# Performance work log

Measured on AMD Instinct MI355X. Metric: run time of the kernel, lower is better.

The kernel has to match this reference:

```python
import jax, jax.numpy as jnp
import numpy as np

B, C, H, W, NH = 8, 192, 128, 128, 6  # batch, channels, height, width, heads


def setup_inputs() -> dict:
    key = jax.random.key(0)
    ks = jax.random.split(key, 5)
    return {
        "x": jax.random.normal(ks[0], (B, C, H, W), jnp.float32),
        "w_qkv": jax.random.normal(ks[1], (3 * C, 1, 3, 3), jnp.float32) * 0.1,  # grouped conv, groups=C
        "b_qkv": jax.random.normal(ks[2], (3 * C,), jnp.float32) * 0.1,
        "temperature": jnp.ones((NH, 1, 1), jnp.float32),
        "w_out": jax.random.normal(ks[3], (C, C), jnp.float32) * 0.05,  # 1x1 conv as dense
        "b_out": jax.random.normal(ks[4], (C,), jnp.float32) * 0.05,
    }


def reference(x, w_qkv, b_qkv, temperature, w_out, b_out):
    b, c, h, w = x.shape
    nh = temperature.shape[0]
    # grouped 3x3 conv (groups = in_ch), padding=1
    qkv = jax.lax.conv_general_dilated(
        x, w_qkv, window_strides=(1, 1), padding=[(1, 1), (1, 1)],
        feature_group_count=c, dimension_numbers=("NCHW", "OIHW", "NCHW"),
    ) + b_qkv[None, :, None, None]
    q, k, v = jnp.split(qkv, 3, axis=1)  # each [b, c, h, w]

    def to_heads(t):
        return t.reshape(b, nh, c // nh, h * w)  # b head c (h w)

    q, k, v = to_heads(q), to_heads(k), to_heads(v)
    eps = 1e-12  # F.normalize default
    q = q / jnp.maximum(jnp.linalg.norm(q, axis=-1, keepdims=True), eps)
    k = k / jnp.maximum(jnp.linalg.norm(k, axis=-1, keepdims=True), eps)
    attn = jnp.einsum("bhcn,bhdn->bhcd", q, k) * temperature[None]  # [b, nh, c/nh, c/nh]
    attn = jax.nn.softmax(attn, axis=-1)
    out = jnp.einsum("bhcd,bhdn->bhcn", attn, v).reshape(b, c, h, w)
    out = jnp.einsum("oc,bchw->bohw", w_out, out) + b_out[None, :, None, None]
    return out
```

## Files before the change

kernel.cpp:

```cpp
#include <hip/hip_runtime.h>
#include <hip/hip_bf16.h>

constexpr int B   = 8;
constexpr int Cc  = 192;
constexpr int H   = 128;
constexpr int Wd  = 128;
constexpr int NH  = 6;
constexpr int HW  = H * Wd;
constexpr int QKV = 3 * Cc;

typedef short s16x4 __attribute__((ext_vector_type(4)));
typedef short s16x8 __attribute__((ext_vector_type(8)));
typedef float f32x16 __attribute__((ext_vector_type(16)));

constexpr size_t OFF_QKV  = 0;
constexpr size_t OFF_ATTN = 150994944ULL;
constexpr size_t OFF_SSQ  = OFF_ATTN + 196608ULL;
constexpr size_t OFF_M    = OFF_SSQ + 12288ULL;
constexpr int    N_ZERO   = (196608 + 12288) / 4;

__device__ inline unsigned short f2bf(float f) {
    __hip_bfloat16 h = __float2bfloat16(f);
    return *(unsigned short*)&h;
}

__global__ void zero_kernel(float* __restrict__ p, int n) {
    int i = blockIdx.x * 256 + threadIdx.x;
    if (i < n) p[i] = 0.f;
}

constexpr int TS = 16;

__global__ __launch_bounds__(256) void conv_qkv(
    const float* __restrict__ x, const float* __restrict__ w,
    const float* __restrict__ bias, unsigned short* __restrict__ qkv,
    float* __restrict__ ssq)
{
    int tile = blockIdx.x;
    int g    = blockIdx.y;
    int b    = blockIdx.z;
    int tid  = threadIdx.x;
    int y    = tile * TS + (tid >> 4);
    int xq   = (tid & 15) * 8;

    const float* xp = x + ((size_t)b * Cc + g) * HW;

    float r[3][10];
    for (int dr = 0; dr < 3; ++dr) {
        int yy = y - 1 + dr;
        bool vy = (yy >= 0) && (yy < H);
        const float* rp = xp + (size_t)yy * Wd;
        if (vy) {
            float4 a4 = *(const float4*)(rp + xq);
            float4 b4 = *(const float4*)(rp + xq + 4);
            r[dr][0] = (xq > 0)   ? rp[xq - 1] : 0.f;
            r[dr][1] = a4.x; r[dr][2] = a4.y; r[dr][3] = a4.z; r[dr][4] = a4.w;
            r[dr][5] = b4.x; r[dr][6] = b4.y; r[dr][7] = b4.z; r[dr][8] = b4.w;
            r[dr][9] = (xq < 120) ? rp[xq + 8] : 0.f;
        } else {
            for (int i = 0; i < 10; ++i) r[dr][i] = 0.f;
        }
    }

    float wreg[3][9], breg[3];
    for (int j = 0; j < 3; ++j) {
        const float* wp = w + (size_t)(3 * g + j) * 9;
        for (int t = 0; t < 9; ++t) wreg[j][t] = wp[t];
        breg[j] = bias[3 * g + j];
    }

    bool track = (g < 128);
    float ss[3] = {0.f, 0.f, 0.f};

    for (int j = 0; j < 3; ++j) {
        unsigned short pk[8];
        for (int xx = 0; xx < 8; ++xx) {
            float s = breg[j];
            for (int dr = 0; dr < 3; ++dr)
                s += wreg[j][dr * 3 + 0] * r[dr][xx]
                   + wreg[j][dr * 3 + 1] * r[dr][xx + 1]
                   + wreg[j][dr * 3 + 2] * r[dr][xx + 2];
            if (track) ss[j] += s * s;
            pk[xx] = f2bf(s);
        }
        unsigned short* op = qkv + ((size_t)b * QKV + 3 * g + j) * HW
                                 + (size_t)y * Wd + xq;
        uint4 uu;
        uu.x = (unsigned int)pk[0] | ((unsigned int)pk[1] << 16);
        uu.y = (unsigned int)pk[2] | ((unsigned int)pk[3] << 16);
        uu.z = (unsigned int)pk[4] | ((unsigned int)pk[5] << 16);
        uu.w = (unsigned int)pk[6] | ((unsigned int)pk[7] << 16);
        *(uint4*)op = uu;
    }

    if (track) {
        __shared__ float red[256];
        for (int j = 0; j < 3; ++j) {
            red[tid] = ss[j];
            __syncthreads();
            for (int st = 128; st > 0; st >>= 1) {
                if (tid < st) red[tid] += red[tid + st];
                __syncthreads();
            }
            if (tid == 0) {
                int o = 3 * g + j;
                atomicAdd(&ssq[(o < Cc ? 0 : 1) * B * Cc + b * Cc + (o % Cc)], red[0]);
            }
            __syncthreads();
        }
    }
}

constexpr int NSEG = 64;
constexpr int SEGN = HW / NSEG;

__global__ __launch_bounds__(256) void qk_mfma(
    const unsigned short* __restrict__ qkv, float* __restrict__ attn)
{
    int h = blockIdx.y, b = blockIdx.z;
    int tid = threadIdx.x;
    int wv = tid >> 6, lane = tid & 63;
    int seg = blockIdx.x * 4 + wv;
    int col = lane & 31, half = lane >> 5;

    __shared__ float sred[4][1024];

    const unsigned short* qp = qkv + ((size_t)b * QKV + h * 32 + col) * HW
                                   + seg * SEGN + half * 8;
    const unsigned short* kp = qp + (size_t)Cc * HW;

    f32x16 acc0, acc1;
    for (int i = 0; i < 16; ++i) { acc0[i] = 0.f; acc1[i] = 0.f; }

    for (int kk = 0; kk < SEGN; kk += 32) {
        s16x8 a0 = *(const s16x8*)(qp + kk);
        s16x8 b0 = *(const s16x8*)(kp + kk);
        acc0 = __builtin_amdgcn_mfma_f32_32x32x16_bf16(a0, b0, acc0, 0, 0, 0);
        s16x8 a1 = *(const s16x8*)(qp + kk + 16);
        s16x8 b1 = *(const s16x8*)(kp + kk + 16);
        acc1 = __builtin_amdgcn_mfma_f32_32x32x16_bf16(a1, b1, acc1, 0, 0, 0);
    }

    int rb = half * 4;
    for (int r = 0; r < 16; ++r) {
        int row = (r & 3) + 8 * (r >> 2) + rb;
        sred[wv][row * 32 + col] = acc0[r] + acc1[r];
    }
    __syncthreads();
    float* ap = attn + (size_t)(b * NH + h) * 1024;
    for (int i = tid; i < 1024; i += 256)
        atomicAdd(&ap[i], sred[0][i] + sred[1][i] + sred[2][i] + sred[3][i]);
}

__global__ void softmax_attn(float* __restrict__ attn,
                             const float* __restrict__ ssq,
                             const float* __restrict__ temp)
{
    int h = blockIdx.x % NH, b = blockIdx.x / NH;
    __shared__ float nk[32];
    if (threadIdx.x < 32)
        nk[threadIdx.x] = fmaxf(sqrtf(ssq[B * Cc + b * Cc + h * 32 + threadIdx.x]), 1e-12f);
    __syncthreads();
    int c = threadIdx.x;
    if (c >= 32) return;
    float nq = fmaxf(sqrtf(ssq[b * Cc + h * 32 + c]), 1e-12f);
    float t = temp[h];
    float* ap = attn + ((size_t)(b * NH + h) * 32 + c) * 32;
    float row[32];
    float mx = -1e30f;
    for (int d = 0; d < 32; ++d) {
        float v = ap[d] / (nq * nk[d]) * t;
        row[d] = v;
        mx = fmaxf(mx, v);
    }
    float sum = 0.f;
    for (int d = 0; d < 32; ++d) { row[d] = expf(row[d] - mx); sum += row[d]; }
    float inv = 1.f / sum;
    for (int d = 0; d < 32; ++d) ap[d] = row[d] * inv;
}

__global__ __launch_bounds__(256) void make_m(
    const float* __restrict__ attn, const float* __restrict__ w_out,
    unsigned short* __restrict__ M)
{
    int h = blockIdx.x, b = blockIdx.y;
    __shared__ float as[32][33];
    for (int i = threadIdx.x; i < 1024; i += 256)
        as[i / 32][i % 32] = attn[(size_t)((b * NH + h) * 32 + i / 32) * 32 + i % 32];
    __syncthreads();
    for (int i = threadIdx.x; i < Cc * 32; i += 256) {
        int o = i / 32, d = i % 32;
        const float* wp = w_out + (size_t)o * Cc + h * 32;
        float s = 0.f;
        for (int cp = 0; cp < 32; ++cp) s += wp[cp] * as[cp][d];
        M[((size_t)b * Cc + o) * Cc + h * 32 + d] = f2bf(s);
    }
}

constexpr int BN = 128;

__global__ __launch_bounds__(256) void out_gemm(
    const unsigned short* __restrict__ M, const unsigned short* __restrict__ qkv,
    const float* __restrict__ b_out, float* __restrict__ out)
{
    int tid  = threadIdx.x;
    int wv   = tid >> 6, lane = tid & 63;
    int b    = blockIdx.y;
    int n0   = blockIdx.x * BN + wv * 32;
    int col  = lane & 31, half = lane >> 5;
    int a    = lane >> 3;
    int bq   = lane & 7;

    __shared__ unsigned short vsT[4][32][20];
    unsigned short (*vt)[20] = vsT[wv];

    const unsigned short* vp = qkv + ((size_t)b * QKV + 2 * Cc) * HW + n0 + 4 * bq;
    const unsigned short* mp = M + (size_t)b * Cc * Cc;

    f32x16 acc[6];
    for (int t = 0; t < 6; ++t)
        for (int i = 0; i < 16; ++i) acc[t][i] = 0.f;

    const unsigned short* s0 = vp + (size_t)(2 * a) * HW;
    ushort4 va = *(const ushort4*)s0;
    ushort4 vb = *(const ushort4*)(s0 + HW);

    for (int k0 = 0; k0 < Cc; k0 += 16) {
        *(unsigned int*)&vt[4 * bq + 0][2 * a] = (unsigned int)va.x | ((unsigned int)vb.x << 16);
        *(unsigned int*)&vt[4 * bq + 1][2 * a] = (unsigned int)va.y | ((unsigned int)vb.y << 16);
        *(unsigned int*)&vt[4 * bq + 2][2 * a] = (unsigned int)va.z | ((unsigned int)vb.z << 16);
        *(unsigned int*)&vt[4 * bq + 3][2 * a] = (unsigned int)va.w | ((unsigned int)vb.w << 16);
        if (k0 + 16 < Cc) {
            const unsigned short* s1 = vp + (size_t)(k0 + 16 + 2 * a) * HW;
            va = *(const ushort4*)s1;
            vb = *(const ushort4*)(s1 + HW);
        }
        __builtin_amdgcn_wave_barrier();
        s16x4 lo = *(const s16x4*)&vt[col][half * 8];
        s16x4 hi = *(const s16x4*)&vt[col][half * 8 + 4];
        s16x8 bf = __builtin_shufflevector(lo, hi, 0, 1, 2, 3, 4, 5, 6, 7);
        for (int mt = 0; mt < 6; ++mt) {
            s16x8 af = *(const s16x8*)(mp + (size_t)(mt * 32 + col) * Cc + k0 + half * 8);
            acc[mt] = __builtin_amdgcn_mfma_f32_32x32x16_bf16(af, bf, acc[mt], 0, 0, 0);
        }
        __builtin_amdgcn_wave_barrier();
    }

    for (int mt = 0; mt < 6; ++mt) {
        f32x16 c = acc[mt];
        for (int rr = 0; rr < 16; ++rr) {
            int row = (rr & 3) + 8 * (rr >> 2) + 4 * half;
            int o = mt * 32 + row;
            out[((size_t)b * Cc + o) * HW + n0 + col] = c[rr] + b_out[o];
        }
    }
}

extern "C" void kernel_launch(void* const* d_in, const int* in_sizes, int n_in,
                              void* d_out, int out_size, void* d_ws, size_t ws_size,
                              hipStream_t stream) {
    const float* x      = (const float*)d_in[0];
    const float* w_qkv  = (const float*)d_in[1];
    const float* b_qkv  = (const float*)d_in[2];
    const float* temp   = (const float*)d_in[3];
    const float* w_out  = (const float*)d_in[4];
    const float* b_out  = (const float*)d_in[5];
    float* out = (float*)d_out;

    char* ws = (char*)d_ws;
    unsigned short* qkv = (unsigned short*)(ws + OFF_QKV);
    float* attn         = (float*)(ws + OFF_ATTN);
    float* ssq          = (float*)(ws + OFF_SSQ);
    unsigned short* M   = (unsigned short*)(ws + OFF_M);

    zero_kernel<<<(N_ZERO + 255) / 256, 256, 0, stream>>>(attn, N_ZERO);
    conv_qkv<<<dim3(H / TS, Cc, B), 256, 0, stream>>>(x, w_qkv, b_qkv, qkv, ssq);
    qk_mfma<<<dim3(NSEG / 4, NH, B), 256, 0, stream>>>(qkv, attn);
    softmax_attn<<<B * NH, 64, 0, stream>>>(attn, ssq, temp);
    make_m<<<dim3(NH, B), 256, 0, stream>>>(attn, w_out, M);
    out_gemm<<<dim3(HW / BN, B), 256, 0, stream>>>(M, qkv, b_out, out);
}
```

Measured before the change: 298.9 us.

## Stage conv input in shared memory and replace QK atomics with partial buffers

The depthwise conv now loads a haloed 18x128 tile into shared memory with coalesced float4 loads and gets the left and right neighbour columns through lane shuffles. The sum-of-squares reduction switches from a shared-memory tree with many barriers to wavefront shuffle reductions, with one atomic per wave. The QK^T kernel stages Q and K chunks in LDS with coalesced loads and writes per-partition partial results instead of atomics, and softmax sums the 8 partials. This adds a barrier per chunk in the QK kernel and cuts its grid to 8 blocks per (b,h), which may reduce parallelism.

```diff
diff --git a/kernel.cpp b/kernel.cpp
--- a/kernel.cpp
+++ b/kernel.cpp
@@ -14,10 +14,11 @@
 typedef float f32x16 __attribute__((ext_vector_type(16)));
 
 constexpr size_t OFF_QKV  = 0;
-constexpr size_t OFF_ATTN = 150994944ULL;
+constexpr size_t OFF_PART = 150994944ULL;
+constexpr size_t OFF_ATTN = OFF_PART + 1572864ULL;
 constexpr size_t OFF_SSQ  = OFF_ATTN + 196608ULL;
 constexpr size_t OFF_M    = OFF_SSQ + 12288ULL;
-constexpr int    N_ZERO   = (196608 + 12288) / 4;
+constexpr int    N_ZERO   = 12288 / 4;
 
 __device__ inline unsigned short f2bf(float f) {
     __hip_bfloat16 h = __float2bfloat16(f);
@@ -40,26 +41,17 @@
     int g    = blockIdx.y;
     int b    = blockIdx.z;
     int tid  = threadIdx.x;
-    int y    = tile * TS + (tid >> 4);
-    int xq   = (tid & 15) * 8;
+    int y0   = tile * TS;
+
+    __shared__ float smx[TS + 2][132];
 
     const float* xp = x + ((size_t)b * Cc + g) * HW;
-
-    float r[3][10];
-    for (int dr = 0; dr < 3; ++dr) {
-        int yy = y - 1 + dr;
-        bool vy = (yy >= 0) && (yy < H);
-        const float* rp = xp + (size_t)yy * Wd;
-        if (vy) {
-            float4 a4 = *(const float4*)(rp + xq);
-            float4 b4 = *(const float4*)(rp + xq + 4);
-            r[dr][0] = (xq > 0)   ? rp[xq - 1] : 0.f;
-            r[dr][1] = a4.x; r[dr][2] = a4.y; r[dr][3] = a4.z; r[dr][4] = a4.w;
-            r[dr][5] = b4.x; r[dr][6] = b4.y; r[dr][7] = b4.z; r[dr][8] = b4.w;
-            r[dr][9] = (xq < 120) ? rp[xq + 8] : 0.f;
-        } else {
-            for (int i = 0; i < 10; ++i) r[dr][i] = 0.f;
-        }
+    for (int i = tid; i < (TS + 2) * 32; i += 256) {
+        int r = i >> 5, c4 = (i & 31) * 4;
+        int y = y0 - 1 + r;
+        float4 v4 = make_float4(0.f, 0.f, 0.f, 0.f);
+        if (y >= 0 && y < H) v4 = *(const float4*)(xp + (size_t)y * Wd + c4);
+        *(float4*)&smx[r][c4] = v4;
     }
 
     float wreg[3][9], breg[3];
@@ -68,19 +60,41 @@
         for (int t = 0; t < 9; ++t) wreg[j][t] = wp[t];
         breg[j] = bias[3 * g + j];
     }
+    __syncthreads();
+
+    int yy = tid >> 4;
+    int xi = tid & 15;
+    int xq = xi * 8;
+
+    float acc[3][8];
+    for (int j = 0; j < 3; ++j)
+        for (int xx = 0; xx < 8; ++xx) acc[j][xx] = breg[j];
+
+    for (int dr = 0; dr < 3; ++dr) {
+        float4 a4 = *(const float4*)&smx[yy + dr][xq];
+        float4 b4 = *(const float4*)&smx[yy + dr][xq + 4];
+        float l = __shfl_up(b4.w, 1);
+        float rr = __shfl_down(a4.x, 1);
+        float wd[10];
+        wd[0] = (xi == 0) ? 0.f : l;
+        wd[1] = a4.x; wd[2] = a4.y; wd[3] = a4.z; wd[4] = a4.w;
+        wd[5] = b4.x; wd[6] = b4.y; wd[7] = b4.z; wd[8] = b4.w;
+        wd[9] = (xi == 15) ? 0.f : rr;
+        for (int j = 0; j < 3; ++j) {
+            float w0 = wreg[j][dr * 3], w1 = wreg[j][dr * 3 + 1], w2 = wreg[j][dr * 3 + 2];
+            for (int xx = 0; xx < 8; ++xx)
+                acc[j][xx] += w0 * wd[xx] + w1 * wd[xx + 1] + w2 * wd[xx + 2];
+        }
+    }
 
     bool track = (g < 128);
-    float ss[3] = {0.f, 0.f, 0.f};
-
+    int y = y0 + yy;
     for (int j = 0; j < 3; ++j) {
+        float ss = 0.f;
         unsigned short pk[8];
         for (int xx = 0; xx < 8; ++xx) {
-            float s = breg[j];
-            for (int dr = 0; dr < 3; ++dr)
-                s += wreg[j][dr * 3 + 0] * r[dr][xx]
-                   + wreg[j][dr * 3 + 1] * r[dr][xx + 1]
-                   + wreg[j][dr * 3 + 2] * r[dr][xx + 2];
-            if (track) ss[j] += s * s;
+            float s = acc[j][xx];
+            ss += s * s;
             pk[xx] = f2bf(s);
         }
         unsigned short* op = qkv + ((size_t)b * QKV + 3 * g + j) * HW
@@ -91,68 +105,71 @@
         uu.z = (unsigned int)pk[4] | ((unsigned int)pk[5] << 16);
         uu.w = (unsigned int)pk[6] | ((unsigned int)pk[7] << 16);
         *(uint4*)op = uu;
-    }
-
-    if (track) {
-        __shared__ float red[256];
-        for (int j = 0; j < 3; ++j) {
-            red[tid] = ss[j];
-            __syncthreads();
-            for (int st = 128; st > 0; st >>= 1) {
-                if (tid < st) red[tid] += red[tid + st];
-                __syncthreads();
+        if (track) {
+            for (int off = 1; off < 64; off <<= 1) ss += __shfl_xor(ss, off);
+            if ((tid & 63) == 0) {
+                int o = 3 * g + j;
+                atomicAdd(&ssq[(o < Cc ? 0 : 1) * B * Cc + b * Cc + (o % Cc)], ss);
             }
-            if (tid == 0) {
-                int o = 3 * g + j;
-                atomicAdd(&ssq[(o < Cc ? 0 : 1) * B * Cc + b * Cc + (o % Cc)], red[0]);
-            }
-            __syncthreads();
-        }
-    }
-}
-
-constexpr int NSEG = 64;
-constexpr int SEGN = HW / NSEG;
+        }
+    }
+}
+
+constexpr int NPART = 8;
 
 __global__ __launch_bounds__(256) void qk_mfma(
-    const unsigned short* __restrict__ qkv, float* __restrict__ attn)
+    const unsigned short* __restrict__ qkv, float* __restrict__ part)
 {
     int h = blockIdx.y, b = blockIdx.z;
     int tid = threadIdx.x;
     int wv = tid >> 6, lane = tid & 63;
-    int seg = blockIdx.x * 4 + wv;
     int col = lane & 31, half = lane >> 5;
 
-    __shared__ float sred[4][1024];
-
-    const unsigned short* qp = qkv + ((size_t)b * QKV + h * 32 + col) * HW
-                                   + seg * SEGN + half * 8;
-    const unsigned short* kp = qp + (size_t)Cc * HW;
-
-    f32x16 acc0, acc1;
-    for (int i = 0; i < 16; ++i) { acc0[i] = 0.f; acc1[i] = 0.f; }
-
-    for (int kk = 0; kk < SEGN; kk += 32) {
-        s16x8 a0 = *(const s16x8*)(qp + kk);
-        s16x8 b0 = *(const s16x8*)(kp + kk);
-        acc0 = __builtin_amdgcn_mfma_f32_32x32x16_bf16(a0, b0, acc0, 0, 0, 0);
-        s16x8 a1 = *(const s16x8*)(qp + kk + 16);
-        s16x8 b1 = *(const s16x8*)(kp + kk + 16);
-        acc1 = __builtin_amdgcn_mfma_f32_32x32x16_bf16(a1, b1, acc1, 0, 0, 0);
-    }
-
-    int rb = half * 4;
+    __shared__ unsigned short qs[32][264];
+    __shared__ unsigned short ks[32][264];
+
+    const unsigned short* qb = qkv + ((size_t)b * QKV + h * 32) * HW
+                                   + (size_t)blockIdx.x * (HW / NPART);
+    const unsigned short* kb = qb + (size_t)Cc * HW;
+
+    f32x16 acc;
+    for (int i = 0; i < 16; ++i) acc[i] = 0.f;
+
+    for (int chunk = 0; chunk < 8; ++chunk) {
+        int nc = chunk * 256;
+        for (int it = 0; it < 8; ++it) {
+            int idx = it * 256 + tid;
+            int row = idx >> 5, ch = idx & 31;
+            const unsigned short* src = (row < 32 ? qb + (size_t)row * HW
+                                                  : kb + (size_t)(row - 32) * HW)
+                                        + nc + ch * 8;
+            uint4 d = *(const uint4*)src;
+            unsigned short* dst = (row < 32) ? &qs[row][ch * 8] : &ks[row - 32][ch * 8];
+            *(uint4*)dst = d;
+        }
+        __syncthreads();
+        int koff = wv * 64 + half * 8;
+        for (int t = 0; t < 4; ++t) {
+            s16x8 a = *(const s16x8*)&qs[col][koff + t * 16];
+            s16x8 bb = *(const s16x8*)&ks[col][koff + t * 16];
+            acc = __builtin_amdgcn_mfma_f32_32x32x16_bf16(a, bb, acc, 0, 0, 0);
+        }
+        __syncthreads();
+    }
+
+    float* sred = (float*)&qs[0][0];
     for (int r = 0; r < 16; ++r) {
-        int row = (r & 3) + 8 * (r >> 2) + rb;
-        sred[wv][row * 32 + col] = acc0[r] + acc1[r];
+        int row = (r & 3) + 8 * (r >> 2) + 4 * half;
+        sred[wv * 1024 + row * 32 + col] = acc[r];
     }
     __syncthreads();
-    float* ap = attn + (size_t)(b * NH + h) * 1024;
+    float* pp = part + (((size_t)(b * NH + h)) * NPART + blockIdx.x) * 1024;
     for (int i = tid; i < 1024; i += 256)
-        atomicAdd(&ap[i], sred[0][i] + sred[1][i] + sred[2][i] + sred[3][i]);
-}
-
-__global__ void softmax_attn(float* __restrict__ attn,
+        pp[i] = sred[i] + sred[1024 + i] + sred[2048 + i] + sred[3072 + i];
+}
+
+__global__ void softmax_attn(const float* __restrict__ part,
+                             float* __restrict__ attn,
                              const float* __restrict__ ssq,
                              const float* __restrict__ temp)
 {
@@ -165,17 +182,20 @@
     if (c >= 32) return;
     float nq = fmaxf(sqrtf(ssq[b * Cc + h * 32 + c]), 1e-12f);
     float t = temp[h];
-    float* ap = attn + ((size_t)(b * NH + h) * 32 + c) * 32;
+    const float* pp = part + (size_t)(b * NH + h) * (NPART * 1024) + c * 32;
     float row[32];
     float mx = -1e30f;
     for (int d = 0; d < 32; ++d) {
-        float v = ap[d] / (nq * nk[d]) * t;
+        float v = 0.f;
+        for (int p = 0; p < NPART; ++p) v += pp[p * 1024 + d];
+        v = v / (nq * nk[d]) * t;
         row[d] = v;
         mx = fmaxf(mx, v);
     }
     float sum = 0.f;
     for (int d = 0; d < 32; ++d) { row[d] = expf(row[d] - mx); sum += row[d]; }
     float inv = 1.f / sum;
+    float* ap = attn + ((size_t)(b * NH + h) * 32 + c) * 32;
     for (int d = 0; d < 32; ++d) ap[d] = row[d] * inv;
 }
 
@@ -269,14 +289,15 @@
 
     char* ws = (char*)d_ws;
     unsigned short* qkv = (unsigned short*)(ws + OFF_QKV);
+    float* part         = (float*)(ws + OFF_PART);
     float* attn         = (float*)(ws + OFF_ATTN);
     float* ssq          = (float*)(ws + OFF_SSQ);
     unsigned short* M   = (unsigned short*)(ws + OFF_M);
 
-    zero_kernel<<<(N_ZERO + 255) / 256, 256, 0, stream>>>(attn, N_ZERO);
+    zero_kernel<<<(N_ZERO + 255) / 256, 256, 0, stream>>>(ssq, N_ZERO);
     conv_qkv<<<dim3(H / TS, Cc, B), 256, 0, stream>>>(x, w_qkv, b_qkv, qkv, ssq);
-    qk_mfma<<<dim3(NSEG / 4, NH, B), 256, 0, stream>>>(qkv, attn);
-    softmax_attn<<<B * NH, 64, 0, stream>>>(attn, ssq, temp);
+    qk_mfma<<<dim3(NPART, NH, B), 256, 0, stream>>>(qkv, part);
+    softmax_attn<<<B * NH, 64, 0, stream>>>(part, attn, ssq, temp);
     make_m<<<dim3(NH, B), 256, 0, stream>>>(attn, w_out, M);
     out_gemm<<<dim3(HW / BN, B), 256, 0, stream>>>(M, qkv, b_out, out);
 }
```

Result: slower. 316.4 us (+5.9%).
